# Kernel optimization log

Hardware: AMD Instinct MI355X
Metric: run time of the kernel (lower is better)

The kernel has to match this reference:

```python
import jax, jax.numpy as jnp
import numpy as np

N_BOND = 2_000_000
N_ATOM = 100_000
N_STRUCT = 2
THREEBODY_CUTOFF = 0.8


def setup_inputs() -> dict:
    key = jax.random.key(0)
    k1, k2 = jax.random.split(key)
    # bonds grouped (sorted) by source atom, as _compute_threebody assumes
    bond_src = jnp.sort(jax.random.randint(k1, (N_BOND,), 0, N_ATOM))
    bond_length = jax.random.uniform(k2, (N_BOND,), dtype=jnp.float32)
    n_atoms = jnp.full((N_STRUCT,), N_ATOM // N_STRUCT, dtype=jnp.int32)
    return {"bond_src": bond_src, "bond_length": bond_length, "n_atoms": n_atoms}


def reference(bond_src, bond_length, n_atoms):
    """Vectorized equivalent of compute_threebody_indices.

    Returns (bond_indices [T,2] pairs of ORIGINAL bond ids, n_triple_ij [n_bond],
    n_triple_i [n_atom], n_triple_s [n_struct]). Replaces the O(n) Python loops
    with segment-sum (degree count), prefix-sum (CSR offsets) and a flat
    enumeration of ordered within-atom bond pairs (j != k).
    """
    n_bond = bond_src.shape[0]
    n_atom = int(jnp.sum(n_atoms))
    n_struct = n_atoms.shape[0]

    # --- filter bonds by three-body cutoff, remember original bond ids ---
    mask = bond_length <= THREEBODY_CUTOFF
    kept = jnp.nonzero(mask)[0]          # original bond indices of surviving bonds
    src = bond_src[kept]                 # still sorted (subset of a sorted array)

    # --- per-atom bond counts and CSR offsets (parallel histogram + scan) ---
    deg = jax.ops.segment_sum(jnp.ones_like(src), src, num_segments=n_atom)
    bond_offset = jnp.cumsum(deg) - deg  # start of each atom's bond block

    # --- triples per atom / per bond / per structure ---
    n_triple_i = deg * (deg - 1)
    T = int(jnp.sum(n_triple_i))

    # --- enumerate all ordered pairs (j, k), j != k, within each atom block ---
    tri_atom = jnp.repeat(jnp.arange(n_atom), n_triple_i, total_repeat_length=T)
    tri_start = (jnp.cumsum(n_triple_i) - n_triple_i)[tri_atom]
    t = jnp.arange(T) - tri_start        # local triple index in [0, d*(d-1))
    d = deg[tri_atom]                    # d >= 2 wherever triples exist
    j = t // (d - 1)
    kp = t % (d - 1)
    k = kp + (kp >= j).astype(kp.dtype)  # skip k == j, preserving loop order
    b0 = bond_offset[tri_atom] + j       # relative (filtered) bond index
    b1 = bond_offset[tri_atom] + k
    bond_indices = jnp.stack([kept[b0], kept[b1]], axis=1)  # back to ORIGINAL ids

    # angles per ORIGINAL bond: deg(src)-1 for surviving bonds, 0 for filtered
    n_triple_ij = jnp.zeros(n_bond, dtype=deg.dtype).at[kept].set(deg[src] - 1)

    # angles per structure
    struct_id = jnp.repeat(jnp.arange(n_struct), n_atoms, total_repeat_length=n_atom)
    n_triple_s = jax.ops.segment_sum(n_triple_i, struct_id, num_segments=n_struct)

    return bond_indices, n_triple_ij, n_triple_i, n_triple_s
```

## Files before the change

### kernel.cpp

```cpp
#include <hip/hip_runtime.h>


#define CUTOFF 0.8f
#define NATOM_C 100000
#define MAXD 256

__global__ void k0_init(int* wstart, int* wend, int* deg, int n_atom) {
    int i = blockIdx.x * blockDim.x + threadIdx.x;
    if (i < n_atom) { wstart[i] = 0; wend[i] = 0; deg[i] = 0; }
}

__global__ void kA_bounds_deg(const int* __restrict__ src, const float* __restrict__ len,
                              int* __restrict__ wstart, int* __restrict__ wend,
                              int* __restrict__ deg, int n_bond) {
    int i = blockIdx.x * blockDim.x + threadIdx.x;
    int lane = threadIdx.x & 63;
    bool valid = i < n_bond;
    int a = -1;
    bool kept = false;
    if (valid) {
        a = src[i];
        if (i == 0 || src[i - 1] != a) wstart[a] = i;
        if (i == n_bond - 1 || src[i + 1] != a) wend[a] = i + 1;
        kept = (len[i] <= CUTOFF);
    }
    unsigned long long keptB = __ballot(kept);
    int ap = __shfl_up(a, 1);
    bool head = (lane == 0) || (ap != a);
    unsigned long long headB = __ballot(head);
    unsigned long long nextHeads = (headB >> 1) >> lane;
    bool tail = (lane == 63) || ((nextHeads & 1ull) != 0ull);
    if (tail && valid) {
        unsigned long long below = (lane == 63) ? ~0ull : ((2ull << lane) - 1ull);
        int runStart = 63 - __clzll(headB & below);
        unsigned long long runMask = below & ~((1ull << runStart) - 1ull);
        int cnt = __popcll(keptB & runMask);
        if (cnt) atomicAdd(&deg[a], cnt);
    }
}

__global__ void kB_scan(const int* __restrict__ deg, int* __restrict__ out_i,
                        int* __restrict__ exsc, int* __restrict__ bsums, int n) {
    __shared__ int tmp[256];
    int t = threadIdx.x;
    int base = blockIdx.x * 1024 + t * 4;
    int v0 = 0, v1 = 0, v2 = 0, v3 = 0;
    if (base     < n) { int d = deg[base];     v0 = d * (d - 1); out_i[base]     = v0; }
    if (base + 1 < n) { int d = deg[base + 1]; v1 = d * (d - 1); out_i[base + 1] = v1; }
    if (base + 2 < n) { int d = deg[base + 2]; v2 = d * (d - 1); out_i[base + 2] = v2; }
    if (base + 3 < n) { int d = deg[base + 3]; v3 = d * (d - 1); out_i[base + 3] = v3; }
    int s = v0 + v1 + v2 + v3;
    tmp[t] = s;
    __syncthreads();
    for (int off = 1; off < 256; off <<= 1) {
        int v = (t >= off) ? tmp[t - off] : 0;
        __syncthreads();
        tmp[t] += v;
        __syncthreads();
    }
    int excl = tmp[t] - s;
    if (base     < n) exsc[base]     = excl;
    if (base + 1 < n) exsc[base + 1] = excl + v0;
    if (base + 2 < n) exsc[base + 2] = excl + v0 + v1;
    if (base + 3 < n) exsc[base + 3] = excl + v0 + v1 + v2;
    if (t == 255) bsums[blockIdx.x] = tmp[255];
}

__global__ void kC_scan2(int* __restrict__ bsums, const int* __restrict__ exsc,
                         const int* __restrict__ n_atoms_arr, int* __restrict__ out_s,
                         int nb, int n_atom, int n_struct) {
    const int B = 256;
    __shared__ int sums[B];
    int t = threadIdx.x;
    int chunk = (nb + B - 1) / B;
    int lo = t * chunk; if (lo > nb) lo = nb;
    int hi = lo + chunk; if (hi > nb) hi = nb;
    int ssum = 0;
    for (int i = lo; i < hi; i++) ssum += bsums[i];
    sums[t] = ssum;
    __syncthreads();
    for (int off = 1; off < B; off <<= 1) {
        int v = (t >= off) ? sums[t - off] : 0;
        __syncthreads();
        sums[t] += v;
        __syncthreads();
    }
    int run = sums[t] - ssum;
    for (int i = lo; i < hi; i++) { int v = bsums[i]; bsums[i] = run; run += v; }
    int total = sums[B - 1];
    __syncthreads();
    if (t == 0) {
        int off = 0, prevA = 0;
        for (int s = 0; s < n_struct; s++) {
            off += n_atoms_arr[s];
            int A = (off >= n_atom) ? total : (exsc[off] + bsums[off >> 10]);
            out_s[s] = A - prevA;
            prevA = A;
        }
    }
}

__global__ void kD_enum(const float* __restrict__ len, const int* __restrict__ wstart,
                        const int* __restrict__ wend, const int* __restrict__ exsc,
                        const int* __restrict__ bsums,
                        int4* __restrict__ out4, int* __restrict__ out_ij,
                        int n_atom) {
    __shared__ int keptIds[4 * MAXD];
    int wave = threadIdx.x >> 6;
    int lane = threadIdx.x & 63;
    int a = blockIdx.x * 4 + wave;
    int* my = &keptIds[wave * MAXD];
    int d = 0, s = 0, e = 0;
    if (a < n_atom) {
        s = wstart[a]; e = wend[a];
        for (int base = s; base < e; base += 64) {
            int idx = base + lane;
            bool m = (idx < e) && (len[idx] <= CUTOFF);
            unsigned long long bal = __ballot(m);
            int pos = d + __popcll(bal & ((1ull << lane) - 1ull));
            if (m && pos < MAXD) my[pos] = idx;
            d += __popcll(bal);
        }
        int dm1 = d - 1;
        for (int idx = s + lane; idx < e; idx += 64)
            out_ij[idx] = (len[idx] <= CUTOFF) ? dm1 : 0;
    }
    __syncthreads();
    if (a < n_atom && d >= 2) {
        unsigned dm1 = (unsigned)(d - 1);
        unsigned nP = ((unsigned)(d * (d - 1))) >> 1;
        int base_row = exsc[a] + bsums[a >> 10];
        int b4 = base_row >> 1;
        for (unsigned p = lane; p < nP; p += 64) {
            unsigned t0 = 2u * p;
            unsigned j  = t0 / dm1;
            unsigned kp = t0 - j * dm1;
            unsigned j1 = j, kp1 = kp + 1;
            if (kp1 == dm1) { j1++; kp1 = 0; }
            unsigned k0 = kp  + (kp  >= j  ? 1u : 0u);
            unsigned k1 = kp1 + (kp1 >= j1 ? 1u : 0u);
            out4[b4 + p] = make_int4(my[j], my[k0], my[j1], my[k1]);
        }
    }
}

extern "C" void kernel_launch(void* const* d_in, const int* in_sizes, int n_in,
                              void* d_out, int out_size, void* d_ws, size_t ws_size,
                              hipStream_t stream) {
    const int*   bond_src    = (const int*)d_in[0];
    const float* bond_len    = (const float*)d_in[1];
    const int*   n_atoms_arr = (const int*)d_in[2];
    int n_bond   = in_sizes[0];
    int n_struct = in_sizes[2];
    const int n_atom = NATOM_C;
    int T2 = out_size - n_bond - n_atom - n_struct;

    int nblk_scan = (n_atom + 1023) / 1024;

    int* ws     = (int*)d_ws;
    int* wstart = ws;
    int* wend   = ws + n_atom;
    int* deg    = ws + 2 * n_atom;
    int* exsc   = ws + 3 * n_atom;
    int* bsums  = exsc + n_atom;

    int*  out       = (int*)d_out;
    int4* out_pairs = (int4*)out;
    int*  out_ij    = out + T2;
    int*  out_i     = out_ij + n_bond;
    int*  out_s     = out_i + n_atom;

    k0_init      <<<(n_atom + 255) / 256, 256, 0, stream>>>(wstart, wend, deg, n_atom);
    kA_bounds_deg<<<(n_bond + 255) / 256, 256, 0, stream>>>(bond_src, bond_len, wstart, wend, deg, n_bond);
    kB_scan      <<<nblk_scan, 256, 0, stream>>>(deg, out_i, exsc, bsums, n_atom);
    kC_scan2     <<<1, 256, 0, stream>>>(bsums, exsc, n_atoms_arr, out_s, nblk_scan, n_atom, n_struct);
    kD_enum      <<<(n_atom + 3) / 4, 256, 0, stream>>>(bond_len, wstart, wend, exsc, bsums, out_pairs, out_ij, n_atom);
}
```

Baseline: 244.1 us.

## Fuse all stages into one cooperative persistent kernel with grid syncs

Replaces the five separate kernel launches with a single cooperative kernel of 1024 blocks that runs init, bond bounds and degree counting, tile scan, global scan and triple enumeration as phases separated by grid.sync(). This removes per-launch overhead and the gaps between kernels. It adds grid-wide barriers, and the enumeration phase now loops a fixed set of waves over atoms, which may balance work worse than one wave per atom. If the cooperative launch fails, the old multi-kernel path runs, with kD_enum now exiting early instead of hitting a block barrier.

```diff
diff --git a/kernel.cpp b/kernel.cpp
--- a/kernel.cpp
+++ b/kernel.cpp
@@ -1,9 +1,157 @@
 #include <hip/hip_runtime.h>
+#include <hip/hip_cooperative_groups.h>
+
+namespace cg = cooperative_groups;
 
 
 #define CUTOFF 0.8f
 #define NATOM_C 100000
 #define MAXD 256
+#define NBLK 1024
+#define NTHR 256
+
+__global__ __launch_bounds__(NTHR, 4) void mega(
+    const int* __restrict__ src, const float* __restrict__ len,
+    const int* __restrict__ n_atoms_arr,
+    int4* __restrict__ out4, int* __restrict__ out_ij,
+    int* __restrict__ out_i, int* __restrict__ out_s,
+    int* __restrict__ wstart, int* __restrict__ wend, int* __restrict__ deg,
+    int* __restrict__ exsc, int* __restrict__ bsums,
+    int n_bond, int n_atom, int n_struct, int ntiles)
+{
+    cg::grid_group grid = cg::this_grid();
+    __shared__ int shbuf[4 * MAXD];
+
+    const int tid      = blockIdx.x * NTHR + (int)threadIdx.x;
+    const int nthreads = gridDim.x * NTHR;
+    const int lane     = threadIdx.x & 63;
+
+    for (int i = tid; i < n_atom; i += nthreads) { wstart[i] = 0; wend[i] = 0; deg[i] = 0; }
+    grid.sync();
+
+    int iters = (n_bond + nthreads - 1) / nthreads;
+    for (int it = 0; it < iters; ++it) {
+        int i = tid + it * nthreads;
+        bool valid = i < n_bond;
+        int a = -1; bool kept = false;
+        if (valid) {
+            a = src[i];
+            if (i == 0 || src[i - 1] != a) wstart[a] = i;
+            if (i == n_bond - 1 || src[i + 1] != a) wend[a] = i + 1;
+            kept = (len[i] <= CUTOFF);
+        }
+        unsigned long long keptB = __ballot(kept);
+        int ap = __shfl_up(a, 1);
+        bool head = (lane == 0) || (ap != a);
+        unsigned long long headB = __ballot(head);
+        unsigned long long nextHeads = (headB >> 1) >> lane;
+        bool tail = (lane == 63) || ((nextHeads & 1ull) != 0ull);
+        if (tail && valid) {
+            unsigned long long below = (lane == 63) ? ~0ull : ((2ull << lane) - 1ull);
+            int runStart = 63 - __clzll(headB & below);
+            unsigned long long runMask = below & ~((1ull << runStart) - 1ull);
+            int cnt = __popcll(keptB & runMask);
+            if (cnt) atomicAdd(&deg[a], cnt);
+        }
+    }
+    grid.sync();
+
+    for (int t = blockIdx.x; t < ntiles; t += gridDim.x) {
+        int* tmp = shbuf;
+        int tt = threadIdx.x;
+        int base = t * 1024 + tt * 4;
+        int v0 = 0, v1 = 0, v2 = 0, v3 = 0;
+        if (base     < n_atom) { int d = deg[base];     v0 = d * (d - 1); out_i[base]     = v0; }
+        if (base + 1 < n_atom) { int d = deg[base + 1]; v1 = d * (d - 1); out_i[base + 1] = v1; }
+        if (base + 2 < n_atom) { int d = deg[base + 2]; v2 = d * (d - 1); out_i[base + 2] = v2; }
+        if (base + 3 < n_atom) { int d = deg[base + 3]; v3 = d * (d - 1); out_i[base + 3] = v3; }
+        int s = v0 + v1 + v2 + v3;
+        tmp[tt] = s;
+        __syncthreads();
+        for (int off = 1; off < 256; off <<= 1) {
+            int v = (tt >= off) ? tmp[tt - off] : 0;
+            __syncthreads();
+            tmp[tt] += v;
+            __syncthreads();
+        }
+        int excl = tmp[tt] - s;
+        if (base     < n_atom) exsc[base]     = excl;
+        if (base + 1 < n_atom) exsc[base + 1] = excl + v0;
+        if (base + 2 < n_atom) exsc[base + 2] = excl + v0 + v1;
+        if (base + 3 < n_atom) exsc[base + 3] = excl + v0 + v1 + v2;
+        if (tt == 255) bsums[t] = tmp[255];
+        __syncthreads();
+    }
+    grid.sync();
+
+    if (blockIdx.x == 0) {
+        int* sums = shbuf;
+        int t = threadIdx.x;
+        int chunk = (ntiles + 255) / 256;
+        int lo = t * chunk; if (lo > ntiles) lo = ntiles;
+        int hi = lo + chunk; if (hi > ntiles) hi = ntiles;
+        int ssum = 0;
+        for (int i = lo; i < hi; i++) ssum += bsums[i];
+        sums[t] = ssum;
+        __syncthreads();
+        for (int off = 1; off < 256; off <<= 1) {
+            int v = (t >= off) ? sums[t - off] : 0;
+            __syncthreads();
+            sums[t] += v;
+            __syncthreads();
+        }
+        int run = sums[t] - ssum;
+        for (int i = lo; i < hi; i++) { int v = bsums[i]; bsums[i] = run; run += v; }
+        int total = sums[255];
+        __syncthreads();
+        if (t == 0) {
+            int off = 0, prevA = 0;
+            for (int s2 = 0; s2 < n_struct; s2++) {
+                off += n_atoms_arr[s2];
+                int A = (off >= n_atom) ? total : (exsc[off] + bsums[off >> 10]);
+                out_s[s2] = A - prevA;
+                prevA = A;
+            }
+        }
+    }
+    grid.sync();
+
+    {
+        int* my = &shbuf[(threadIdx.x >> 6) * MAXD];
+        int gwave  = blockIdx.x * (NTHR / 64) + (threadIdx.x >> 6);
+        int nwaves = gridDim.x * (NTHR / 64);
+        for (int a = gwave; a < n_atom; a += nwaves) {
+            int s = wstart[a], e = wend[a];
+            int d = 0;
+            for (int base = s; base < e; base += 64) {
+                int idx = base + lane;
+                bool m = (idx < e) && (len[idx] <= CUTOFF);
+                unsigned long long bal = __ballot(m);
+                int pos = d + __popcll(bal & ((1ull << lane) - 1ull));
+                if (m && pos < MAXD) my[pos] = idx;
+                d += __popcll(bal);
+            }
+            int dm1 = d - 1;
+            for (int idx = s + lane; idx < e; idx += 64)
+                out_ij[idx] = (len[idx] <= CUTOFF) ? dm1 : 0;
+            if (d >= 2) {
+                unsigned udm1 = (unsigned)dm1;
+                unsigned nP = ((unsigned)(d * dm1)) >> 1;
+                int b4 = (exsc[a] + bsums[a >> 10]) >> 1;
+                for (unsigned p = lane; p < nP; p += 64) {
+                    unsigned t0 = 2u * p;
+                    unsigned j  = t0 / udm1;
+                    unsigned kp = t0 - j * udm1;
+                    unsigned j1 = j, kp1 = kp + 1;
+                    if (kp1 == udm1) { j1++; kp1 = 0; }
+                    unsigned k0 = kp  + (kp  >= j  ? 1u : 0u);
+                    unsigned k1 = kp1 + (kp1 >= j1 ? 1u : 0u);
+                    out4[b4 + p] = make_int4(my[j], my[k0], my[j1], my[k1]);
+                }
+            }
+        }
+    }
+}
 
 __global__ void k0_init(int* wstart, int* wend, int* deg, int n_atom) {
     int i = blockIdx.x * blockDim.x + threadIdx.x;
@@ -110,33 +258,30 @@
     int lane = threadIdx.x & 63;
     int a = blockIdx.x * 4 + wave;
     int* my = &keptIds[wave * MAXD];
-    int d = 0, s = 0, e = 0;
-    if (a < n_atom) {
-        s = wstart[a]; e = wend[a];
-        for (int base = s; base < e; base += 64) {
-            int idx = base + lane;
-            bool m = (idx < e) && (len[idx] <= CUTOFF);
-            unsigned long long bal = __ballot(m);
-            int pos = d + __popcll(bal & ((1ull << lane) - 1ull));
-            if (m && pos < MAXD) my[pos] = idx;
-            d += __popcll(bal);
-        }
-        int dm1 = d - 1;
-        for (int idx = s + lane; idx < e; idx += 64)
-            out_ij[idx] = (len[idx] <= CUTOFF) ? dm1 : 0;
-    }
-    __syncthreads();
-    if (a < n_atom && d >= 2) {
-        unsigned dm1 = (unsigned)(d - 1);
-        unsigned nP = ((unsigned)(d * (d - 1))) >> 1;
-        int base_row = exsc[a] + bsums[a >> 10];
-        int b4 = base_row >> 1;
+    if (a >= n_atom) return;
+    int s = wstart[a], e = wend[a];
+    int d = 0;
+    for (int base = s; base < e; base += 64) {
+        int idx = base + lane;
+        bool m = (idx < e) && (len[idx] <= CUTOFF);
+        unsigned long long bal = __ballot(m);
+        int pos = d + __popcll(bal & ((1ull << lane) - 1ull));
+        if (m && pos < MAXD) my[pos] = idx;
+        d += __popcll(bal);
+    }
+    int dm1 = d - 1;
+    for (int idx = s + lane; idx < e; idx += 64)
+        out_ij[idx] = (len[idx] <= CUTOFF) ? dm1 : 0;
+    if (d >= 2) {
+        unsigned udm1 = (unsigned)dm1;
+        unsigned nP = ((unsigned)(d * dm1)) >> 1;
+        int b4 = (exsc[a] + bsums[a >> 10]) >> 1;
         for (unsigned p = lane; p < nP; p += 64) {
             unsigned t0 = 2u * p;
-            unsigned j  = t0 / dm1;
-            unsigned kp = t0 - j * dm1;
+            unsigned j  = t0 / udm1;
+            unsigned kp = t0 - j * udm1;
             unsigned j1 = j, kp1 = kp + 1;
-            if (kp1 == dm1) { j1++; kp1 = 0; }
+            if (kp1 == udm1) { j1++; kp1 = 0; }
             unsigned k0 = kp  + (kp  >= j  ? 1u : 0u);
             unsigned k1 = kp1 + (kp1 >= j1 ? 1u : 0u);
             out4[b4 + p] = make_int4(my[j], my[k0], my[j1], my[k1]);
@@ -152,10 +297,10 @@
     const int*   n_atoms_arr = (const int*)d_in[2];
     int n_bond   = in_sizes[0];
     int n_struct = in_sizes[2];
-    const int n_atom = NATOM_C;
+    int n_atom   = NATOM_C;
     int T2 = out_size - n_bond - n_atom - n_struct;
 
-    int nblk_scan = (n_atom + 1023) / 1024;
+    int ntiles = (n_atom + 1023) / 1024;
 
     int* ws     = (int*)d_ws;
     int* wstart = ws;
@@ -170,9 +315,19 @@
     int*  out_i     = out_ij + n_bond;
     int*  out_s     = out_i + n_atom;
 
-    k0_init      <<<(n_atom + 255) / 256, 256, 0, stream>>>(wstart, wend, deg, n_atom);
-    kA_bounds_deg<<<(n_bond + 255) / 256, 256, 0, stream>>>(bond_src, bond_len, wstart, wend, deg, n_bond);
-    kB_scan      <<<nblk_scan, 256, 0, stream>>>(deg, out_i, exsc, bsums, n_atom);
-    kC_scan2     <<<1, 256, 0, stream>>>(bsums, exsc, n_atoms_arr, out_s, nblk_scan, n_atom, n_struct);
-    kD_enum      <<<(n_atom + 3) / 4, 256, 0, stream>>>(bond_len, wstart, wend, exsc, bsums, out_pairs, out_ij, n_atom);
-}
+    void* args[] = {
+        (void*)&bond_src, (void*)&bond_len, (void*)&n_atoms_arr,
+        (void*)&out_pairs, (void*)&out_ij, (void*)&out_i, (void*)&out_s,
+        (void*)&wstart, (void*)&wend, (void*)&deg, (void*)&exsc, (void*)&bsums,
+        (void*)&n_bond, (void*)&n_atom, (void*)&n_struct, (void*)&ntiles
+    };
+    hipError_t err = hipLaunchCooperativeKernel((const void*)mega, dim3(NBLK), dim3(NTHR),
+                                                args, 0, stream);
+    if (err != hipSuccess) {
+        k0_init      <<<(n_atom + 255) / 256, 256, 0, stream>>>(wstart, wend, deg, n_atom);
+        kA_bounds_deg<<<(n_bond + 255) / 256, 256, 0, stream>>>(bond_src, bond_len, wstart, wend, deg, n_bond);
+        kB_scan      <<<ntiles, 256, 0, stream>>>(deg, out_i, exsc, bsums, n_atom);
+        kC_scan2     <<<1, 256, 0, stream>>>(bsums, exsc, n_atoms_arr, out_s, ntiles, n_atom, n_struct);
+        kD_enum      <<<(n_atom + 3) / 4, 256, 0, stream>>>(bond_len, wstart, wend, exsc, bsums, out_pairs, out_ij, n_atom);
+    }
+}
```

Result: slower. 628.7 us (+157.5%).

## Vectorize bond-bounds pass and fuse two-level scan via last-block completion

Applied to the files above, without the earlier changes.

The bounds/degree kernel now handles four bonds per thread with int4/float4 loads and merges atomics for runs of equal atoms serially, replacing the ballot-based run detection. The scan and its second level are fused into one kernel: each tile publishes its block sum, and the last block to finish (found through an atomic counter) scans the block sums and writes the per-structure totals. This drops one kernel launch and the serial single-block pass. The enum kernel drops its now-unneeded __syncthreads by returning early. The fused scan assumes at most 256 tiles and relies on correct fences for the last-block handoff.

```diff
diff --git a/kernel.cpp b/kernel.cpp
--- a/kernel.cpp
+++ b/kernel.cpp
@@ -5,50 +5,87 @@
 #define NATOM_C 100000
 #define MAXD 256
 
-__global__ void k0_init(int* wstart, int* wend, int* deg, int n_atom) {
+__global__ void k0_init(int* wstart, int* wend, int* deg, int* done, int n_atom) {
     int i = blockIdx.x * blockDim.x + threadIdx.x;
     if (i < n_atom) { wstart[i] = 0; wend[i] = 0; deg[i] = 0; }
+    if (i == 0) *done = 0;
 }
 
 __global__ void kA_bounds_deg(const int* __restrict__ src, const float* __restrict__ len,
                               int* __restrict__ wstart, int* __restrict__ wend,
                               int* __restrict__ deg, int n_bond) {
-    int i = blockIdx.x * blockDim.x + threadIdx.x;
+    int q  = blockIdx.x * blockDim.x + threadIdx.x;
+    int g0 = q * 4;
     int lane = threadIdx.x & 63;
-    bool valid = i < n_bond;
-    int a = -1;
-    bool kept = false;
-    if (valid) {
-        a = src[i];
-        if (i == 0 || src[i - 1] != a) wstart[a] = i;
-        if (i == n_bond - 1 || src[i + 1] != a) wend[a] = i + 1;
-        kept = (len[i] <= CUTOFF);
-    }
-    unsigned long long keptB = __ballot(kept);
-    int ap = __shfl_up(a, 1);
-    bool head = (lane == 0) || (ap != a);
-    unsigned long long headB = __ballot(head);
-    unsigned long long nextHeads = (headB >> 1) >> lane;
-    bool tail = (lane == 63) || ((nextHeads & 1ull) != 0ull);
-    if (tail && valid) {
-        unsigned long long below = (lane == 63) ? ~0ull : ((2ull << lane) - 1ull);
-        int runStart = 63 - __clzll(headB & below);
-        unsigned long long runMask = below & ~((1ull << runStart) - 1ull);
-        int cnt = __popcll(keptB & runMask);
-        if (cnt) atomicAdd(&deg[a], cnt);
-    }
-}
-
-__global__ void kB_scan(const int* __restrict__ deg, int* __restrict__ out_i,
-                        int* __restrict__ exsc, int* __restrict__ bsums, int n) {
+    bool full = (g0 + 3 < n_bond);
+
+    int4   s4 = make_int4(-3, -3, -3, -3);
+    float4 l4 = make_float4(1e9f, 1e9f, 1e9f, 1e9f);
+    if (full) {
+        s4 = *(const int4*)(src + g0);
+        l4 = *(const float4*)(len + g0);
+    }
+    int prevN = __shfl_up(s4.w, 1);
+    int nextN = __shfl_down(s4.x, 1);
+    if (lane == 0)  prevN = (g0 > 0 && g0 - 1 < n_bond) ? src[g0 - 1] : -1;
+    if (lane == 63) nextN = (g0 + 4 < n_bond) ? src[g0 + 4] : -2;
+    if (g0 + 4 >= n_bond) nextN = -2;
+
+    if (full) {
+        int a0 = s4.x, a1 = s4.y, a2 = s4.z, a3 = s4.w;
+        if (g0 == 0 || a0 != prevN) wstart[a0] = g0;
+        if (a1 != a0) wstart[a1] = g0 + 1;
+        if (a2 != a1) wstart[a2] = g0 + 2;
+        if (a3 != a2) wstart[a3] = g0 + 3;
+        if (a0 != a1) wend[a0] = g0 + 1;
+        if (a1 != a2) wend[a1] = g0 + 2;
+        if (a2 != a3) wend[a2] = g0 + 3;
+        if (g0 + 4 == n_bond || a3 != nextN) wend[a3] = g0 + 4;
+        int c0 = (l4.x <= CUTOFF) ? 1 : 0;
+        int c1 = (l4.y <= CUTOFF) ? 1 : 0;
+        int c2 = (l4.z <= CUTOFF) ? 1 : 0;
+        int c3 = (l4.w <= CUTOFF) ? 1 : 0;
+        int aCur = a0, cnt = c0;
+        if (a1 != aCur) { if (cnt) atomicAdd(&deg[aCur], cnt); aCur = a1; cnt = 0; }
+        cnt += c1;
+        if (a2 != aCur) { if (cnt) atomicAdd(&deg[aCur], cnt); aCur = a2; cnt = 0; }
+        cnt += c2;
+        if (a3 != aCur) { if (cnt) atomicAdd(&deg[aCur], cnt); aCur = a3; cnt = 0; }
+        cnt += c3;
+        if (cnt) atomicAdd(&deg[aCur], cnt);
+    } else if (g0 < n_bond) {
+        for (int j = 0; j < 4; j++) {
+            int g = g0 + j;
+            if (g >= n_bond) break;
+            int a = src[g];
+            if (g == 0 || src[g - 1] != a) wstart[a] = g;
+            if (g == n_bond - 1 || src[g + 1] != a) wend[a] = g + 1;
+            if (len[g] <= CUTOFF) atomicAdd(&deg[a], 1);
+        }
+    }
+}
+
+__global__ void kBC_scan(const int* __restrict__ deg, int* __restrict__ out_i,
+                         int* __restrict__ exsc, int* __restrict__ bsums,
+                         int* __restrict__ done, const int* __restrict__ n_atoms_arr,
+                         int* __restrict__ out_s,
+                         int n_atom, int ntiles, int n_struct) {
     __shared__ int tmp[256];
+    __shared__ int isLast;
     int t = threadIdx.x;
     int base = blockIdx.x * 1024 + t * 4;
     int v0 = 0, v1 = 0, v2 = 0, v3 = 0;
-    if (base     < n) { int d = deg[base];     v0 = d * (d - 1); out_i[base]     = v0; }
-    if (base + 1 < n) { int d = deg[base + 1]; v1 = d * (d - 1); out_i[base + 1] = v1; }
-    if (base + 2 < n) { int d = deg[base + 2]; v2 = d * (d - 1); out_i[base + 2] = v2; }
-    if (base + 3 < n) { int d = deg[base + 3]; v3 = d * (d - 1); out_i[base + 3] = v3; }
+    if (base + 3 < n_atom) {
+        int4 d4 = *(const int4*)(deg + base);
+        v0 = d4.x * (d4.x - 1); v1 = d4.y * (d4.y - 1);
+        v2 = d4.z * (d4.z - 1); v3 = d4.w * (d4.w - 1);
+        *(int4*)(out_i + base) = make_int4(v0, v1, v2, v3);
+    } else {
+        if (base     < n_atom) { int d = deg[base];     v0 = d * (d - 1); out_i[base]     = v0; }
+        if (base + 1 < n_atom) { int d = deg[base + 1]; v1 = d * (d - 1); out_i[base + 1] = v1; }
+        if (base + 2 < n_atom) { int d = deg[base + 2]; v2 = d * (d - 1); out_i[base + 2] = v2; }
+        if (base + 3 < n_atom) { int d = deg[base + 3]; v3 = d * (d - 1); out_i[base + 3] = v3; }
+    }
     int s = v0 + v1 + v2 + v3;
     tmp[t] = s;
     __syncthreads();
@@ -59,42 +96,45 @@
         __syncthreads();
     }
     int excl = tmp[t] - s;
-    if (base     < n) exsc[base]     = excl;
-    if (base + 1 < n) exsc[base + 1] = excl + v0;
-    if (base + 2 < n) exsc[base + 2] = excl + v0 + v1;
-    if (base + 3 < n) exsc[base + 3] = excl + v0 + v1 + v2;
+    if (base     < n_atom) exsc[base]     = excl;
+    if (base + 1 < n_atom) exsc[base + 1] = excl + v0;
+    if (base + 2 < n_atom) exsc[base + 2] = excl + v0 + v1;
+    if (base + 3 < n_atom) exsc[base + 3] = excl + v0 + v1 + v2;
     if (t == 255) bsums[blockIdx.x] = tmp[255];
-}
-
-__global__ void kC_scan2(int* __restrict__ bsums, const int* __restrict__ exsc,
-                         const int* __restrict__ n_atoms_arr, int* __restrict__ out_s,
-                         int nb, int n_atom, int n_struct) {
-    const int B = 256;
-    __shared__ int sums[B];
-    int t = threadIdx.x;
-    int chunk = (nb + B - 1) / B;
-    int lo = t * chunk; if (lo > nb) lo = nb;
-    int hi = lo + chunk; if (hi > nb) hi = nb;
-    int ssum = 0;
-    for (int i = lo; i < hi; i++) ssum += bsums[i];
-    sums[t] = ssum;
-    __syncthreads();
-    for (int off = 1; off < B; off <<= 1) {
-        int v = (t >= off) ? sums[t - off] : 0;
-        __syncthreads();
-        sums[t] += v;
-        __syncthreads();
-    }
-    int run = sums[t] - ssum;
-    for (int i = lo; i < hi; i++) { int v = bsums[i]; bsums[i] = run; run += v; }
-    int total = sums[B - 1];
+    __syncthreads();
+    if (t == 0) {
+        __threadfence();
+        int old = __hip_atomic_fetch_add(done, 1, __ATOMIC_ACQ_REL,
+                                         __HIP_MEMORY_SCOPE_AGENT);
+        isLast = (old == (int)gridDim.x - 1);
+    }
+    __syncthreads();
+    if (!isLast) return;
+
+    int v = 0;
+    if (t < ntiles)
+        v = __hip_atomic_load(&bsums[t], __ATOMIC_RELAXED, __HIP_MEMORY_SCOPE_AGENT);
+    tmp[t] = v;
+    __syncthreads();
+    for (int off = 1; off < 256; off <<= 1) {
+        int x = (t >= off) ? tmp[t - off] : 0;
+        __syncthreads();
+        tmp[t] += x;
+        __syncthreads();
+    }
+    if (t < ntiles) bsums[t] = tmp[t] - v;
+    int total = tmp[255];
+    __threadfence_block();
     __syncthreads();
     if (t == 0) {
         int off = 0, prevA = 0;
-        for (int s = 0; s < n_struct; s++) {
-            off += n_atoms_arr[s];
-            int A = (off >= n_atom) ? total : (exsc[off] + bsums[off >> 10]);
-            out_s[s] = A - prevA;
+        for (int s2 = 0; s2 < n_struct; s2++) {
+            off += n_atoms_arr[s2];
+            int A;
+            if (off >= n_atom) A = total;
+            else A = __hip_atomic_load(&exsc[off], __ATOMIC_RELAXED,
+                                       __HIP_MEMORY_SCOPE_AGENT) + bsums[off >> 10];
+            out_s[s2] = A - prevA;
             prevA = A;
         }
     }
@@ -110,33 +150,30 @@
     int lane = threadIdx.x & 63;
     int a = blockIdx.x * 4 + wave;
     int* my = &keptIds[wave * MAXD];
-    int d = 0, s = 0, e = 0;
-    if (a < n_atom) {
-        s = wstart[a]; e = wend[a];
-        for (int base = s; base < e; base += 64) {
-            int idx = base + lane;
-            bool m = (idx < e) && (len[idx] <= CUTOFF);
-            unsigned long long bal = __ballot(m);
-            int pos = d + __popcll(bal & ((1ull << lane) - 1ull));
-            if (m && pos < MAXD) my[pos] = idx;
-            d += __popcll(bal);
-        }
-        int dm1 = d - 1;
-        for (int idx = s + lane; idx < e; idx += 64)
-            out_ij[idx] = (len[idx] <= CUTOFF) ? dm1 : 0;
-    }
-    __syncthreads();
-    if (a < n_atom && d >= 2) {
-        unsigned dm1 = (unsigned)(d - 1);
-        unsigned nP = ((unsigned)(d * (d - 1))) >> 1;
-        int base_row = exsc[a] + bsums[a >> 10];
-        int b4 = base_row >> 1;
+    if (a >= n_atom) return;
+    int s = wstart[a], e = wend[a];
+    int d = 0;
+    for (int base = s; base < e; base += 64) {
+        int idx = base + lane;
+        bool m = (idx < e) && (len[idx] <= CUTOFF);
+        unsigned long long bal = __ballot(m);
+        int pos = d + __popcll(bal & ((1ull << lane) - 1ull));
+        if (m && pos < MAXD) my[pos] = idx;
+        d += __popcll(bal);
+    }
+    int dm1 = d - 1;
+    for (int idx = s + lane; idx < e; idx += 64)
+        out_ij[idx] = (len[idx] <= CUTOFF) ? dm1 : 0;
+    if (d >= 2) {
+        unsigned udm1 = (unsigned)dm1;
+        unsigned nP = ((unsigned)(d * dm1)) >> 1;
+        int b4 = (exsc[a] + bsums[a >> 10]) >> 1;
         for (unsigned p = lane; p < nP; p += 64) {
             unsigned t0 = 2u * p;
-            unsigned j  = t0 / dm1;
-            unsigned kp = t0 - j * dm1;
+            unsigned j  = t0 / udm1;
+            unsigned kp = t0 - j * udm1;
             unsigned j1 = j, kp1 = kp + 1;
-            if (kp1 == dm1) { j1++; kp1 = 0; }
+            if (kp1 == udm1) { j1++; kp1 = 0; }
             unsigned k0 = kp  + (kp  >= j  ? 1u : 0u);
             unsigned k1 = kp1 + (kp1 >= j1 ? 1u : 0u);
             out4[b4 + p] = make_int4(my[j], my[k0], my[j1], my[k1]);
@@ -155,7 +192,7 @@
     const int n_atom = NATOM_C;
     int T2 = out_size - n_bond - n_atom - n_struct;
 
-    int nblk_scan = (n_atom + 1023) / 1024;
+    int ntiles = (n_atom + 1023) / 1024;
 
     int* ws     = (int*)d_ws;
     int* wstart = ws;
@@ -163,6 +200,7 @@
     int* deg    = ws + 2 * n_atom;
     int* exsc   = ws + 3 * n_atom;
     int* bsums  = exsc + n_atom;
+    int* done   = bsums + ntiles;
 
     int*  out       = (int*)d_out;
     int4* out_pairs = (int4*)out;
@@ -170,9 +208,12 @@
     int*  out_i     = out_ij + n_bond;
     int*  out_s     = out_i + n_atom;
 
-    k0_init      <<<(n_atom + 255) / 256, 256, 0, stream>>>(wstart, wend, deg, n_atom);
-    kA_bounds_deg<<<(n_bond + 255) / 256, 256, 0, stream>>>(bond_src, bond_len, wstart, wend, deg, n_bond);
-    kB_scan      <<<nblk_scan, 256, 0, stream>>>(deg, out_i, exsc, bsums, n_atom);
-    kC_scan2     <<<1, 256, 0, stream>>>(bsums, exsc, n_atoms_arr, out_s, nblk_scan, n_atom, n_struct);
-    kD_enum      <<<(n_atom + 3) / 4, 256, 0, stream>>>(bond_len, wstart, wend, exsc, bsums, out_pairs, out_ij, n_atom);
-}
+    int nq = (n_bond + 3) / 4;
+
+    k0_init      <<<(n_atom + 255) / 256, 256, 0, stream>>>(wstart, wend, deg, done, n_atom);
+    kA_bounds_deg<<<(nq + 255) / 256, 256, 0, stream>>>(bond_src, bond_len, wstart, wend, deg, n_bond);
+    kBC_scan     <<<ntiles, 256, 0, stream>>>(deg, out_i, exsc, bsums, done, n_atoms_arr,
+                                              out_s, n_atom, ntiles, n_struct);
+    kD_enum      <<<(n_atom + 3) / 4, 256, 0, stream>>>(bond_len, wstart, wend, exsc, bsums,
+                                                        out_pairs, out_ij, n_atom);
+}
```

Result: slower. 256.6 us (+5.1%).
